# Kernel optimization log

Measured on AMD Instinct MI355X. Metric: run time of the kernel, lower is better.

The kernel has to match this reference:

```python
import jax, jax.numpy as jnp
import numpy as np

D_NODE, C, N_HEAD = 256, 32, 8
N_SEQ, N_RES = 256, 256
LN_EPS = 1e-5
MASK_BIAS = 1e9


def setup_inputs() -> dict:
    key = jax.random.key(0)
    ks = jax.random.split(key, 4)
    return {
        "M_raw": jax.random.normal(ks[0], (N_SEQ, N_RES, D_NODE), dtype=jnp.float32),
        "M_mask": jnp.ones((N_SEQ, N_RES), dtype=jnp.float32),
        "ln_w": jnp.ones((D_NODE,), jnp.float32),
        "ln_b": jnp.zeros((D_NODE,), jnp.float32),
        "qkv_w": jax.random.normal(ks[1], (D_NODE, 3 * N_HEAD * C), jnp.float32) * (D_NODE ** -0.5),
        "gate_w": jax.random.normal(ks[2], (D_NODE, N_HEAD * C), jnp.float32) * (D_NODE ** -0.5),
        "gate_b": jnp.ones((N_HEAD * C,), jnp.float32),
        "out_w": jax.random.normal(ks[3], (N_HEAD * C, D_NODE), jnp.float32) * ((N_HEAD * C) ** -0.5),
        "out_b": jnp.zeros((D_NODE,), jnp.float32),
    }


def reference(M_raw, M_mask, ln_w, ln_b, qkv_w, gate_w, gate_b, out_w, out_b):
    # Transpose to column-attention layout: [N_res, N_seq, d]
    M = jnp.swapaxes(M_raw, -2, -3)
    mask = jnp.swapaxes(M_mask, -1, -2)  # [N_res, N_seq]

    # LayerNorm over feature dim
    mu = jnp.mean(M, axis=-1, keepdims=True)
    var = jnp.mean(jnp.square(M - mu), axis=-1, keepdims=True)
    Mn = (M - mu) * jax.lax.rsqrt(var + LN_EPS) * ln_w + ln_b

    # QKV projection (no bias), split heads
    r, s = Mn.shape[0], Mn.shape[1]
    qkv = (Mn @ qkv_w).reshape(r, s, 3, N_HEAD, C)
    q, k, v = qkv[:, :, 0], qkv[:, :, 1], qkv[:, :, 2]  # [r, s, h, c]
    q = q * (C ** -0.5)

    # Masked attention over the sequence (column) axis
    logits = jnp.einsum('rqhc,rkhc->rhqk', q, k)
    logits = logits + (MASK_BIAS * (mask - 1.0))[:, None, None, :]
    weights = jax.nn.softmax(logits, axis=-1)
    o = jnp.einsum('rhqk,rkhc->rqhc', weights, v).reshape(r, s, N_HEAD * C)

    # Sigmoid gating and output projection
    gate = jax.nn.sigmoid(Mn @ gate_w + gate_b)
    out = (o * gate) @ out_w + out_b

    # Residual in original layout
    return M_raw + jnp.swapaxes(out, -2, -3)
```

## Files before the change

kernel.cpp:

```cpp
#include <hip/hip_runtime.h>
#include <hip/hip_bf16.h>


typedef short bf16x8 __attribute__((ext_vector_type(8)));
typedef float f32x4  __attribute__((ext_vector_type(4)));
typedef float f32x16 __attribute__((ext_vector_type(16)));

union U8 { uint w[4]; bf16x8 v; ushort u[8]; };

__device__ __forceinline__ ushort f2bf(float f) {
  uint u = __float_as_uint(f);
  u = (u + 0x7fffu + ((u >> 16) & 1u)) >> 16;
  return (ushort)u;
}

__device__ __forceinline__ uint pk2(float lo, float hi) {
  union { __hip_bfloat162 h; uint u; } cv;
  cv.h = __float22bfloat162_rn(float2{lo, hi});
  return cv.u;
}

__device__ __forceinline__ float exp2fast(float x) {
  return __builtin_amdgcn_exp2f(x);
}

__device__ __forceinline__ f32x16 MFMA32(bf16x8 a, bf16x8 b, f32x16 c) {
  return __builtin_amdgcn_mfma_f32_32x32x16_bf16(a, b, c, 0, 0, 0);
}
__device__ __forceinline__ f32x4 MFMA16(bf16x8 a, bf16x8 b, f32x4 c) {
  return __builtin_amdgcn_mfma_f32_16x16x32_bf16(a, b, c, 0, 0, 0);
}

__device__ __forceinline__ bf16x8 ldG8(const ushort* __restrict__ p, int row, int ko) {
  return *(const bf16x8*)(p + (size_t)row * 256 + ko);
}

__device__ __forceinline__ f32x16 zero16() {
  f32x16 z;
  #pragma unroll
  for (int i = 0; i < 16; ++i) z[i] = 0.f;
  return z;
}

__global__ __launch_bounds__(256) void k_prep(const float* __restrict__ qkv_w,
                                              const float* __restrict__ gate_w,
                                              const float* __restrict__ out_w,
                                              const float* __restrict__ M_mask,
                                              ushort* __restrict__ ws,
                                              uint* __restrict__ mbits) {
  const int b = blockIdx.x;
  const int tid = threadIdx.x;
  if (b == 80) {
    const int r = tid;
    #pragma unroll
    for (int hl = 0; hl < 2; ++hl)
      #pragma unroll
      for (int j = 0; j < 4; ++j) {
        uint m = 0;
        for (int bb = 0; bb < 32; ++bb) {
          const int k0 = j*64 + ((bb>>4)<<5) + (bb&3) + (((bb>>2)&3)<<3) + hl*4;
          m |= (M_mask[(size_t)k0*256 + r] > 0.5f ? 1u : 0u) << bb;
        }
        mbits[(r*2 + hl)*4 + j] = m;
      }
    return;
  }
  __shared__ ushort t[64][72];
  const float* src; ushort* dst; int C, r0, c0; bool scale_q = false;
  if (b < 48)      { src = qkv_w;  dst = ws;          C = 768; r0 = (b/12)*64;      c0 = (b%12)*64; scale_q = true; }
  else if (b < 64) { int bb = b-48; src = gate_w; dst = ws + 196608; C = 256; r0 = (bb>>2)*64; c0 = (bb&3)*64; }
  else             { int bb = b-64; src = out_w;  dst = ws + 262144; C = 256; r0 = (bb>>2)*64; c0 = (bb&3)*64; }
  const int cc = tid & 63, rb = tid >> 6;
  #pragma unroll
  for (int j = 0; j < 16; ++j) {
    const int rr = j*4 + rb;
    float v = src[(size_t)(r0+rr)*C + c0 + cc];
    if (scale_q && (c0+cc) < 256) v *= 0.25503468786609404f;
    t[cc][rr] = f2bf(v);
  }
  __syncthreads();
  const int dd = (tid & 31)*2, cb = tid >> 5;
  #pragma unroll
  for (int j = 0; j < 8; ++j) {
    const int c2 = j*8 + cb;
    const uint wv = (uint)t[c2][dd] | ((uint)t[c2][dd+1] << 16);
    *(uint*)(dst + (size_t)(c0+c2)*256 + r0 + dd) = wv;
  }
}

__global__ __launch_bounds__(256) void k_ln(const float* __restrict__ M_raw,
                                            const float* __restrict__ ln_w,
                                            const float* __restrict__ ln_b,
                                            ushort* __restrict__ Mn) {
  const int s    = blockIdx.x;
  const int rc   = blockIdx.y;
  const int w    = threadIdx.x >> 6;
  const int lane = threadIdx.x & 63;
  const float4 wv = *(const float4*)(ln_w + lane*4);
  const float4 bv = *(const float4*)(ln_b + lane*4);
  const int wofs = (((lane >> 2) << 8) + s) * 16 + (lane & 3) * 4;
  #pragma unroll
  for (int i = 0; i < 8; ++i) {
    const int r = rc*32 + i*4 + w;
    const float4 x = *(const float4*)(M_raw + (size_t)s*65536 + (size_t)r*256 + lane*4);
    float sum = x.x + x.y + x.z + x.w;
    float sq  = x.x*x.x + x.y*x.y + x.z*x.z + x.w*x.w;
    #pragma unroll
    for (int mk = 1; mk <= 32; mk <<= 1) {
      sum += __shfl_xor(sum, mk, 64);
      sq  += __shfl_xor(sq,  mk, 64);
    }
    const float mu = sum * 0.00390625f;
    const float rs = rsqrtf(sq * 0.00390625f - mu*mu + 1e-5f);
    uint2 p2;
    p2.x = pk2((x.x-mu)*rs*wv.x+bv.x, (x.y-mu)*rs*wv.y+bv.y);
    p2.y = pk2((x.z-mu)*rs*wv.z+bv.z, (x.w-mu)*rs*wv.w+bv.w);
    *(uint2*)(Mn + (size_t)r*65536 + wofs) = p2;
  }
}

#define KOFF 0
#define VOFF 20480
#define GOFF 37376

__global__ __launch_bounds__(512, 3) void k_attn(
    const ushort* __restrict__ Mn, const uint* __restrict__ mbits,
    const ushort* __restrict__ qkv_wT, const ushort* __restrict__ gate_wT,
    const float* __restrict__ gate_b, ushort* __restrict__ og)
{
  extern __shared__ char smem[];
  const int bid  = blockIdx.x;
  const int r    = ((bid >> 6) << 3) | (bid & 7);
  const int hd   = (bid >> 3) & 7;
  const int hs   = hd << 5;
  const int tid  = threadIdx.x;
  const int w    = tid >> 6;
  const int lane = tid & 63;
  const int l31  = lane & 31;
  const int hl   = lane >> 5;
  const int Q0   = w << 5;
  const int s    = Q0 + l31;
  const ushort* __restrict__ MnR = Mn + (size_t)r * 65536;

  auto ldMnT = [&](int dt) -> bf16x8 {
    return *(const bf16x8*)(MnR + ((dt << 8) + s) * 16 + hl * 8);
  };

  const uint4 mw4 = *(const uint4*)(mbits + (r*2 + hl)*4);
  const uint m0 = mw4.x, m1 = mw4.y, m2 = mw4.z, m3 = mw4.w;
  const bool full = ((m0 & m1 & m2 & m3) == 0xFFFFFFFFu);

  auto mergeOp = [&](float q0, float q1, float q2, float q3,
                     float q4, float q5, float q6, float q7) -> bf16x8 {
    const uint x0 = pk2(q0, q1), x1 = pk2(q2, q3);
    const uint z0 = pk2(q4, q5), z1 = pk2(q6, q7);
    const uint xx0 = __shfl_xor(x0, 32, 64), xx1 = __shfl_xor(x1, 32, 64);
    const uint zz0 = __shfl_xor(z0, 32, 64), zz1 = __shfl_xor(z1, 32, 64);
    U8 u;
    u.w[0] = hl ? zz0 : x0;
    u.w[1] = hl ? zz1 : x1;
    u.w[2] = hl ? z0  : xx0;
    u.w[3] = hl ? z1  : xx1;
    return u.v;
  };

  auto projT = [&](const ushort* __restrict__ W, int rowbase) -> f32x16 {
    f32x16 a0 = zero16(), a1 = zero16();
    #pragma unroll
    for (int dt = 0; dt < 8; ++dt) {
      a0 = MFMA32(ldG8(W, rowbase + l31, dt*16 + hl*8),     ldMnT(dt),   a0);
      a1 = MFMA32(ldG8(W, rowbase + l31, (dt+8)*16 + hl*8), ldMnT(dt+8), a1);
    }
    return a0 + a1;
  };
  auto projN = [&](const ushort* __restrict__ W, int rowbase) -> f32x16 {
    f32x16 a0 = zero16(), a1 = zero16();
    #pragma unroll
    for (int dt = 0; dt < 8; ++dt) {
      a0 = MFMA32(ldMnT(dt),   ldG8(W, rowbase + l31, dt*16 + hl*8),     a0);
      a1 = MFMA32(ldMnT(dt+8), ldG8(W, rowbase + l31, (dt+8)*16 + hl*8), a1);
    }
    return a0 + a1;
  };
  auto packB = [&](const f32x16& q, bf16x8& lo, bf16x8& hi2) {
    lo  = mergeOp(q[0], q[1], q[2],  q[3],  q[4],  q[5],  q[6],  q[7]);
    hi2 = mergeOp(q[8], q[9], q[10], q[11], q[12], q[13], q[14], q[15]);
  };
  auto stageKV = [&](const f32x16& KA, const f32x16& VA) {
    #pragma unroll
    for (int rq = 0; rq < 4; ++rq) {
      uint2 p2;
      p2.x = pk2(KA[4*rq],   KA[4*rq+1]);
      p2.y = pk2(KA[4*rq+2], KA[4*rq+3]);
      *(uint2*)(smem + KOFF + s*80 + rq*16 + hl*8) = p2;
      p2.x = pk2(VA[4*rq],   VA[4*rq+1]);
      p2.y = pk2(VA[4*rq+2], VA[4*rq+3]);
      *(uint2*)(smem + VOFF + l31*528 + Q0*2 + rq*16 + hl*8) = p2;
    }
  };

  bf16x8 bq0, bq1;
  {
    f32x16 KA = projT(qkv_wT, 256 + hs);
    f32x16 VA = projN(qkv_wT, 512 + hs);
    stageKV(KA, VA);
    f32x16 QA = projT(qkv_wT, hs);
    packB(QA, bq0, bq1);
  }
  __syncthreads();

  float lp0 = 0.f, lp1 = 0.f, lp2 = 0.f, lp3 = 0.f;
  f32x16 Oa = zero16(), Ob = zero16();
  #pragma unroll
  for (int kt = 0; kt < 8; ++kt) {
    const bf16x8 a0 = *(const bf16x8*)(smem + KOFF + (kt*32 + l31)*80 + hl*16);
    const bf16x8 a1 = *(const bf16x8*)(smem + KOFF + (kt*32 + l31)*80 + 32 + hl*16);
    f32x16 S = MFMA32(a0, bq0, zero16());
    S = MFMA32(a1, bq1, S);

    #pragma unroll
    for (int i = 0; i < 16; ++i) {
      float p = exp2fast(S[i]);
      if (!full) {
        const int bi = kt*16 + i;
        const uint mw = (bi < 32) ? m0 : (bi < 64) ? m1 : (bi < 96) ? m2 : m3;
        p = ((mw >> (bi & 31)) & 1u) ? p : 0.f;
      }
      S[i] = p;
      if ((i & 3) == 0) lp0 += p; else if ((i & 3) == 1) lp1 += p;
      else if ((i & 3) == 2) lp2 += p; else lp3 += p;
    }

    const bf16x8 pa0 = mergeOp(S[0], S[1], S[2],  S[3],  S[4],  S[5],  S[6],  S[7]);
    const bf16x8 vb0 = *(const bf16x8*)(smem + VOFF + l31*528 + kt*64 + hl*16);
    Oa = MFMA32(vb0, pa0, Oa);
    const bf16x8 pa1 = mergeOp(S[8], S[9], S[10], S[11], S[12], S[13], S[14], S[15]);
    const bf16x8 vb1 = *(const bf16x8*)(smem + VOFF + l31*528 + kt*64 + 32 + hl*16);
    Ob = MFMA32(vb1, pa1, Ob);
  }
  float l_ = (lp0 + lp1) + (lp2 + lp3);
  l_ += __shfl_xor(l_, 32, 64);
  const float inv = 1.0f / l_;
  const f32x16 O = Oa + Ob;

  f32x16 G = projT(gate_wT, hs);
  const int sxor = (s >> 1) & 15;
  #pragma unroll
  for (int ep = 0; ep < 8; ++ep) {
    const int e0 = 2*ep;
    const int c0 = (e0 & 3) + 8*(e0 >> 2) + 4*hl;
    const float g0 = gate_b[hs + c0];
    const float g1 = gate_b[hs + c0 + 1];
    const float v0 = O[e0]   * inv / (1.f + __expf(-(G[e0]   + g0)));
    const float v1 = O[e0+1] * inv / (1.f + __expf(-(G[e0+1] + g1)));
    const int cpair = (ep & 1) + 4*(ep >> 1) + 2*hl;
    *(uint*)(smem + GOFF + s*64 + ((cpair ^ sxor) << 2)) = pk2(v0, v1);
  }

  __syncthreads();

  uint* ogw = (uint*)og;
  const size_t ob = (size_t)(r*8 + hd) * 4096;
  #pragma unroll
  for (int j = 0; j < 8; ++j) {
    const int lin  = j*512 + tid;
    const int srow = lin >> 4;
    const int cu   = lin & 15;
    const uint wv = *(const uint*)(smem + GOFF + srow*64 + ((cu ^ ((srow >> 1) & 15)) << 2));
    ogw[ob + (size_t)srow*16 + cu] = wv;
  }
}

__global__ __launch_bounds__(256) void k_out(
    const ushort* __restrict__ og, const ushort* __restrict__ out_wT,
    const float* __restrict__ out_b, const float* __restrict__ M_raw,
    float* __restrict__ out)
{
  const int blk  = blockIdx.x;
  const int tid  = threadIdx.x;
  const int w    = tid >> 6;
  const int lane = tid & 63;
  const int l15  = lane & 15;
  const int g    = lane >> 4;
  const int row0 = blk * 64 + w * 16;
  const int r    = row0 >> 8;
  const int s0   = row0 & 255;

  const f32x4 Z = {0.f, 0.f, 0.f, 0.f};
  f32x4 acc[16];
  #pragma unroll
  for (int nt = 0; nt < 16; ++nt) acc[nt] = Z;

  #pragma unroll
  for (int kk = 0; kk < 8; ++kk) {
    const bf16x8 a = *(const bf16x8*)(og + ((size_t)(r*8 + kk)*256 + s0 + l15)*32 + g*8);
    #pragma unroll
    for (int nt = 0; nt < 16; ++nt) {
      const bf16x8 b = ldG8(out_wT, nt*16 + l15, kk*32 + g*8);
      acc[nt] = MFMA16(a, b, acc[nt]);
    }
  }

  #pragma unroll
  for (int nt = 0; nt < 16; ++nt) {
    const int d = nt*16 + l15;
    const float ob = out_b[d];
    #pragma unroll
    for (int i = 0; i < 4; ++i) {
      const int ss = s0 + 4*g + i;
      const size_t idx = (size_t)ss * 65536 + (size_t)r * 256 + d;
      out[idx] = M_raw[idx] + acc[nt][i] + ob;
    }
  }
}

extern "C" void kernel_launch(void* const* d_in, const int* in_sizes, int n_in,
                              void* d_out, int out_size, void* d_ws, size_t ws_size,
                              hipStream_t stream) {
  const float* M_raw  = (const float*)d_in[0];
  const float* M_mask = (const float*)d_in[1];
  const float* ln_w   = (const float*)d_in[2];
  const float* ln_b   = (const float*)d_in[3];
  const float* qkv_w  = (const float*)d_in[4];
  const float* gate_w = (const float*)d_in[5];
  const float* gate_b = (const float*)d_in[6];
  const float* out_w  = (const float*)d_in[7];
  const float* out_b  = (const float*)d_in[8];

  ushort* ws      = (ushort*)d_ws;
  ushort* qkv_wT  = ws;
  ushort* gate_wT = ws + 196608;
  ushort* out_wT  = ws + 262144;
  ushort* og      = ws + 327680;
  ushort* Mn      = ws + 17104896;
  uint*   mbits   = (uint*)(ws + 33882112);

  hipFuncSetAttribute(reinterpret_cast<const void*>(k_attn),
                      hipFuncAttributeMaxDynamicSharedMemorySize, 53760);

  hipLaunchKernelGGL(k_prep, dim3(81), dim3(256), 0, stream,
                     qkv_w, gate_w, out_w, M_mask, ws, mbits);
  hipLaunchKernelGGL(k_ln, dim3(256, 8), dim3(256), 0, stream, M_raw, ln_w, ln_b, Mn);
  hipLaunchKernelGGL(k_attn, dim3(2048), dim3(512), 53760, stream,
                     Mn, mbits, qkv_wT, gate_wT, gate_b, og);
  hipLaunchKernelGGL(k_out, dim3(1024), dim3(256), 0, stream,
                     og, out_wT, out_b, M_raw, (float*)d_out);
}
```

Measured before the change: 414.0 us.

## Cut register pressure in attention kernel to raise occupancy to four blocks

Raises the launch-bounds occupancy hint from 3 to 4 blocks of 512 threads per CU. To fit the tighter register budget, the split dual-accumulator MFMA chains in the projections and the PV product are collapsed into single accumulators, the softmax partial sums drop from four to two, and K and V are projected and staged one at a time rather than both being held live. The aim is more resident waves to hide latency. The cost is longer serial MFMA dependency chains, with less instruction-level parallelism within each wave.

```diff
diff --git a/kernel.cpp b/kernel.cpp
--- a/kernel.cpp
+++ b/kernel.cpp
@@ -123,7 +123,7 @@
 #define VOFF 20480
 #define GOFF 37376
 
-__global__ __launch_bounds__(512, 3) void k_attn(
+__global__ __launch_bounds__(512, 4) void k_attn(
     const ushort* __restrict__ Mn, const uint* __restrict__ mbits,
     const ushort* __restrict__ qkv_wT, const ushort* __restrict__ gate_wT,
     const float* __restrict__ gate_b, ushort* __restrict__ og)
@@ -165,52 +165,53 @@
   };
 
   auto projT = [&](const ushort* __restrict__ W, int rowbase) -> f32x16 {
-    f32x16 a0 = zero16(), a1 = zero16();
-    #pragma unroll
-    for (int dt = 0; dt < 8; ++dt) {
-      a0 = MFMA32(ldG8(W, rowbase + l31, dt*16 + hl*8),     ldMnT(dt),   a0);
-      a1 = MFMA32(ldG8(W, rowbase + l31, (dt+8)*16 + hl*8), ldMnT(dt+8), a1);
-    }
-    return a0 + a1;
+    f32x16 a0 = zero16();
+    #pragma unroll
+    for (int dt = 0; dt < 16; ++dt)
+      a0 = MFMA32(ldG8(W, rowbase + l31, dt*16 + hl*8), ldMnT(dt), a0);
+    return a0;
   };
   auto projN = [&](const ushort* __restrict__ W, int rowbase) -> f32x16 {
-    f32x16 a0 = zero16(), a1 = zero16();
-    #pragma unroll
-    for (int dt = 0; dt < 8; ++dt) {
-      a0 = MFMA32(ldMnT(dt),   ldG8(W, rowbase + l31, dt*16 + hl*8),     a0);
-      a1 = MFMA32(ldMnT(dt+8), ldG8(W, rowbase + l31, (dt+8)*16 + hl*8), a1);
-    }
-    return a0 + a1;
+    f32x16 a0 = zero16();
+    #pragma unroll
+    for (int dt = 0; dt < 16; ++dt)
+      a0 = MFMA32(ldMnT(dt), ldG8(W, rowbase + l31, dt*16 + hl*8), a0);
+    return a0;
   };
   auto packB = [&](const f32x16& q, bf16x8& lo, bf16x8& hi2) {
     lo  = mergeOp(q[0], q[1], q[2],  q[3],  q[4],  q[5],  q[6],  q[7]);
     hi2 = mergeOp(q[8], q[9], q[10], q[11], q[12], q[13], q[14], q[15]);
   };
-  auto stageKV = [&](const f32x16& KA, const f32x16& VA) {
+
+  bf16x8 bq0, bq1;
+  {
+    f32x16 KA = projT(qkv_wT, 256 + hs);
     #pragma unroll
     for (int rq = 0; rq < 4; ++rq) {
       uint2 p2;
       p2.x = pk2(KA[4*rq],   KA[4*rq+1]);
       p2.y = pk2(KA[4*rq+2], KA[4*rq+3]);
       *(uint2*)(smem + KOFF + s*80 + rq*16 + hl*8) = p2;
+    }
+  }
+  {
+    f32x16 VA = projN(qkv_wT, 512 + hs);
+    #pragma unroll
+    for (int rq = 0; rq < 4; ++rq) {
+      uint2 p2;
       p2.x = pk2(VA[4*rq],   VA[4*rq+1]);
       p2.y = pk2(VA[4*rq+2], VA[4*rq+3]);
       *(uint2*)(smem + VOFF + l31*528 + Q0*2 + rq*16 + hl*8) = p2;
     }
-  };
-
-  bf16x8 bq0, bq1;
+  }
   {
-    f32x16 KA = projT(qkv_wT, 256 + hs);
-    f32x16 VA = projN(qkv_wT, 512 + hs);
-    stageKV(KA, VA);
     f32x16 QA = projT(qkv_wT, hs);
     packB(QA, bq0, bq1);
   }
   __syncthreads();
 
-  float lp0 = 0.f, lp1 = 0.f, lp2 = 0.f, lp3 = 0.f;
-  f32x16 Oa = zero16(), Ob = zero16();
+  float lp0 = 0.f, lp1 = 0.f;
+  f32x16 O = zero16();
   #pragma unroll
   for (int kt = 0; kt < 8; ++kt) {
     const bf16x8 a0 = *(const bf16x8*)(smem + KOFF + (kt*32 + l31)*80 + hl*16);
@@ -227,21 +228,19 @@
         p = ((mw >> (bi & 31)) & 1u) ? p : 0.f;
       }
       S[i] = p;
-      if ((i & 3) == 0) lp0 += p; else if ((i & 3) == 1) lp1 += p;
-      else if ((i & 3) == 2) lp2 += p; else lp3 += p;
+      if (i & 1) lp1 += p; else lp0 += p;
     }
 
     const bf16x8 pa0 = mergeOp(S[0], S[1], S[2],  S[3],  S[4],  S[5],  S[6],  S[7]);
     const bf16x8 vb0 = *(const bf16x8*)(smem + VOFF + l31*528 + kt*64 + hl*16);
-    Oa = MFMA32(vb0, pa0, Oa);
+    O = MFMA32(vb0, pa0, O);
     const bf16x8 pa1 = mergeOp(S[8], S[9], S[10], S[11], S[12], S[13], S[14], S[15]);
     const bf16x8 vb1 = *(const bf16x8*)(smem + VOFF + l31*528 + kt*64 + 32 + hl*16);
-    Ob = MFMA32(vb1, pa1, Ob);
-  }
-  float l_ = (lp0 + lp1) + (lp2 + lp3);
+    O = MFMA32(vb1, pa1, O);
+  }
+  float l_ = lp0 + lp1;
   l_ += __shfl_xor(l_, 32, 64);
   const float inv = 1.0f / l_;
-  const f32x16 O = Oa + Ob;
 
   f32x16 G = projT(gate_wT, hs);
   const int sxor = (s >> 1) & 15;
```

Result: no change. 414.0 us (+0.0%).
